# Performance work log

Measured on AMD Instinct MI355X. Metric: run time of the kernel, lower is better.

Reference implementation:

```python
import jax, jax.numpy as jnp
import numpy as np

H, D, Kd, Vd = 16, 1024, 64, 64
N, Mlen = 4096, 4096


def setup_inputs() -> dict:
    key = jax.random.key(0)
    ks = jax.random.split(key, 7)
    X = jax.random.normal(ks[0], (N, D), dtype=jnp.float32)
    M = jax.random.normal(ks[1], (Mlen, D), dtype=jnp.float32)
    mask = jax.random.randint(ks[2], (N, Mlen), 0, 2, dtype=jnp.int32)
    Wq = jax.random.normal(ks[3], (H, D, Kd), dtype=jnp.float32)
    Wk = jax.random.normal(ks[4], (H, D, Kd), dtype=jnp.float32)
    Wv = jax.random.normal(ks[5], (H, D, Vd), dtype=jnp.float32)
    Wo = jax.random.normal(ks[6], (H, Vd, D), dtype=jnp.float32)
    return {"X": X, "M": M, "mask": mask, "Wq": Wq, "Wk": Wk, "Wv": Wv, "Wo": Wo}


def reference(X, M, mask, Wq, Wk, Wv, Wo):
    # Projections: [h,n,k], [h,m,k], [h,m,v]
    Q = jnp.einsum('nd,hdk->hnk', X, Wq)
    K = jnp.einsum('md,hdk->hmk', M, Wk)
    V = jnp.einsum('md,hdv->hmv', M, Wv)
    # Masked attention (no scaling, matching the source)
    logits = jnp.einsum('hnk,hmk->hnm', Q, K)
    logits = jnp.where(mask[None, :, :] == 0, -jnp.inf, logits)
    weights = jax.nn.softmax(logits, axis=-1)
    O = jnp.einsum('hnm,hmv->hnv', weights, V)
    Y = jnp.einsum('hnv,hvd->nd', O, Wo)
    return Y
```

## Files before the change

kernel.cpp:

```cpp
#include <hip/hip_runtime.h>

typedef _Float16 half8 __attribute__((ext_vector_type(8)));
typedef _Float16 half4 __attribute__((ext_vector_type(4)));
typedef __fp16 fp16x2 __attribute__((ext_vector_type(2)));
typedef short short8 __attribute__((ext_vector_type(8)));
typedef short short4v __attribute__((ext_vector_type(4)));
typedef float floatx4 __attribute__((ext_vector_type(4)));

#define LOG2E 1.4426950408889634f

#define GLDS16(g, l) __builtin_amdgcn_global_load_lds( \
    (const __attribute__((address_space(1))) unsigned int*)(g), \
    (__attribute__((address_space(3))) unsigned int*)(l), 16, 0, 0)

static __device__ __forceinline__ short f2bf(float f){
  union { float f; unsigned u; } v; v.f = f;
  unsigned r = v.u + 0x7fffu + ((v.u >> 16) & 1u);
  return (short)(r >> 16);
}
static __device__ __forceinline__ float bf2f(short s){
  union { unsigned u; float f; } v; v.u = ((unsigned)(unsigned short)s) << 16;
  return v.f;
}

__global__ __launch_bounds__(256) void kconvA(const float* __restrict__ X,
                                              const float* __restrict__ Mm,
                                              short* __restrict__ XFh, short* __restrict__ XFl,
                                              short* __restrict__ MFh, short* __restrict__ MFl){
  int b = blockIdx.x;
  int t = threadIdx.x, w = t >> 6, l = t & 63, quad = l >> 4;
  int srcsel = b >> 8, ntile = b & 255;
  const float* A = srcsel ? Mm : X;
  short* oh = srcsel ? MFh : XFh;
  short* ol = srcsel ? MFl : XFl;
  int row = ntile*16 + (l & 15);
  #pragma unroll
  for (int i = 0; i < 8; i++){
    int kt = w*8 + i;
    const float* p = A + (size_t)row*1024 + kt*32 + quad*8;
    float4 v0 = *(const float4*)p, v1 = *(const float4*)(p + 4);
    float vv[8] = {v0.x,v0.y,v0.z,v0.w,v1.x,v1.y,v1.z,v1.w};
    short8 hh, ll;
    #pragma unroll
    for (int j = 0; j < 8; j++){
      short hb = f2bf(vv[j]); hh[j] = hb; ll[j] = f2bf(vv[j] - bf2f(hb));
    }
    size_t off = ((size_t)kt*256 + ntile)*512 + l*8;
    *(short8*)&oh[off] = hh;
    *(short8*)&ol[off] = ll;
  }
}

__global__ __launch_bounds__(256) void kconvW2(const float* __restrict__ Wq,
                                               const float* __restrict__ Wk,
                                               const float* __restrict__ Wv,
                                               short* __restrict__ WFh, short* __restrict__ WFl){
  __shared__ float T[128][68];
  int bidx = blockIdx.x, g = blockIdx.y;
  int mat = bidx >> 4, h = bidx & 15;
  const float* W = (mat == 0 ? Wq : (mat == 1 ? Wk : Wv)) + (size_t)h*65536;
  int t = threadIdx.x, w = t >> 6, l = t & 63, quad = (l >> 4) & 3, fl = l & 15;
  #pragma unroll
  for (int p = 0; p < 32; p++){
    int idx = p*256 + t, row = idx >> 6, col = idx & 63;
    T[row][col] = W[(size_t)(g*128 + row)*64 + col];
  }
  __syncthreads();
  for (int ktl = 0; ktl < 4; ktl++){
    short8 hh, ll;
    #pragma unroll
    for (int j = 0; j < 8; j++){
      float v = T[ktl*32 + quad*8 + j][w*16 + fl];
      short hb = f2bf(v); hh[j] = hb; ll[j] = f2bf(v - bf2f(hb));
    }
    size_t frag = ((size_t)bidx*32 + g*4 + ktl)*4 + w;
    *(short8*)&WFh[frag*512 + l*8] = hh;
    *(short8*)&WFl[frag*512 + l*8] = ll;
  }
}

__global__ __launch_bounds__(256) void kmaskpack(const int* __restrict__ mask,
                                                 unsigned* __restrict__ bits){
  int w = blockIdx.x * 256 + threadIdx.x;
  const int* p = mask + (size_t)w * 32;
  unsigned b = 0;
  #pragma unroll
  for (int i = 0; i < 32; i++) b |= (p[i] != 0) ? (1u << i) : 0u;
  bits[w] = b;
}

__global__ __launch_bounds__(256) void ktransw(const float* __restrict__ src,
                                               short* __restrict__ dsth,
                                               short* __restrict__ dstl,
                                               int R, int C){
  __shared__ float tile[32][33];
  size_t boff = (size_t)blockIdx.z * R * C;
  src += boff; dsth += boff; dstl += boff;
  int r0 = blockIdx.y*32, c0 = blockIdx.x*32;
  int t = threadIdx.x, tr = t >> 3, tc = (t & 7)*4;
  const float* s = src + (size_t)(r0 + tr)*C + c0 + tc;
  #pragma unroll
  for (int i = 0; i < 4; i++) tile[tr][tc + i] = s[i];
  __syncthreads();
  short* dh = dsth + (size_t)(c0 + tr)*R + r0 + tc;
  short* dl = dstl + (size_t)(c0 + tr)*R + r0 + tc;
  #pragma unroll
  for (int i = 0; i < 4; i++){
    float v = tile[tc + i][tr];
    short hb = f2bf(v);
    dh[i] = hb; dl[i] = f2bf(v - bf2f(hb));
  }
}

__global__ __launch_bounds__(256,3) void kproj3(
    const short* __restrict__ XFh, const short* __restrict__ XFl,
    const short* __restrict__ MFh, const short* __restrict__ MFl,
    const short* __restrict__ WFh, const short* __restrict__ WFl,
    _Float16* __restrict__ QFh, _Float16* __restrict__ QFl,
    _Float16* __restrict__ KFh, _Float16* __restrict__ KFl,
    _Float16* __restrict__ VF)
{
  __shared__ short AhL[4096], AlL[4096], BhL[4096], BlL[4096];
  int cb = blockIdx.x, rb = blockIdx.y;
  const bool fused = (cb >= 16);
  int h = fused ? (cb - 16) : cb;
  const short* Ah = fused ? MFh : XFh;
  const short* Al = fused ? MFl : XFl;
  int t = threadIdx.x, w = t >> 6, l = t & 63, quad = l >> 4, ln = l & 15;
  floatx4 acc[2][8] = {};
  for (int kt = 0; kt < 32; kt++){
    __syncthreads();
    size_t abase = ((size_t)kt*256 + rb*8)*512;
    #pragma unroll
    for (int i = 0; i < 2; i++){
      int cidx = i*256 + t;
      GLDS16(Ah + abase + cidx*8, &AhL[(i*256 + w*64)*8]);
      GLDS16(Al + abase + cidx*8, &AlL[(i*256 + w*64)*8]);
    }
    size_t bb0 = (((size_t)cb*32 + kt)*4)*512;
    GLDS16(WFh + bb0 + t*8, &BhL[(w*64)*8]);
    GLDS16(WFl + bb0 + t*8, &BlL[(w*64)*8]);
    if (fused){
      size_t bb1 = (((size_t)(cb + 16)*32 + kt)*4)*512;
      GLDS16(WFh + bb1 + t*8, &BhL[(256 + w*64)*8]);
      GLDS16(WFl + bb1 + t*8, &BlL[(256 + w*64)*8]);
    }
    __syncthreads();
    short8 ah[2], al[2];
    #pragma unroll
    for (int mt = 0; mt < 2; mt++){
      ah[mt] = *(short8*)&AhL[(w*2 + mt)*512 + l*8];
      al[mt] = *(short8*)&AlL[(w*2 + mt)*512 + l*8];
    }
    {
      short8 bh[4], bl[4];
      #pragma unroll
      for (int nt = 0; nt < 4; nt++){
        bh[nt] = *(short8*)&BhL[nt*512 + l*8];
        bl[nt] = *(short8*)&BlL[nt*512 + l*8];
      }
      #pragma unroll
      for (int mt = 0; mt < 2; mt++)
        #pragma unroll
        for (int nt = 0; nt < 4; nt++){
          acc[mt][nt] = __builtin_amdgcn_mfma_f32_16x16x32_bf16(ah[mt], bh[nt], acc[mt][nt], 0, 0, 0);
          acc[mt][nt] = __builtin_amdgcn_mfma_f32_16x16x32_bf16(ah[mt], bl[nt], acc[mt][nt], 0, 0, 0);
          acc[mt][nt] = __builtin_amdgcn_mfma_f32_16x16x32_bf16(al[mt], bh[nt], acc[mt][nt], 0, 0, 0);
        }
    }
    if (fused){
      short8 bh[4], bl[4];
      #pragma unroll
      for (int nt = 0; nt < 4; nt++){
        bh[nt] = *(short8*)&BhL[(4 + nt)*512 + l*8];
        bl[nt] = *(short8*)&BlL[(4 + nt)*512 + l*8];
      }
      #pragma unroll
      for (int mt = 0; mt < 2; mt++)
        #pragma unroll
        for (int nt = 0; nt < 4; nt++){
          acc[mt][4+nt] = __builtin_amdgcn_mfma_f32_16x16x32_bf16(ah[mt], bh[nt], acc[mt][4+nt], 0, 0, 0);
          acc[mt][4+nt] = __builtin_amdgcn_mfma_f32_16x16x32_bf16(ah[mt], bl[nt], acc[mt][4+nt], 0, 0, 0);
          acc[mt][4+nt] = __builtin_amdgcn_mfma_f32_16x16x32_bf16(al[mt], bh[nt], acc[mt][4+nt], 0, 0, 0);
        }
    }
  }
  int row0 = rb*128;
  if (!fused){
    #pragma unroll
    for (int mt = 0; mt < 2; mt++)
      #pragma unroll
      for (int nt = 0; nt < 4; nt++)
        #pragma unroll
        for (int rg = 0; rg < 4; rg++){
          int n = row0 + w*32 + mt*16 + quad*4 + rg;
          int c = nt*16 + ln;
          float v = acc[mt][nt][rg] * LOG2E;
          _Float16 hi = (_Float16)v;
          _Float16 lo = (_Float16)(v - (float)hi);
          int lane2 = (n & 15) + (((c >> 3) & 3) << 4);
          size_t off = (((size_t)h*256 + (n >> 4))*2 + (c >> 5))*512 + lane2*8 + (c & 7);
          QFh[off] = hi; QFl[off] = lo;
        }
  } else {
    #pragma unroll
    for (int mt = 0; mt < 2; mt++)
      #pragma unroll
      for (int nt = 0; nt < 4; nt++)
        #pragma unroll
        for (int rg = 0; rg < 4; rg++){
          int n = row0 + w*32 + mt*16 + quad*4 + rg;
          int c = nt*16 + ln;
          float v = acc[mt][nt][rg];
          _Float16 hi = (_Float16)v;
          _Float16 lo = (_Float16)(v - (float)hi);
          int lane2 = (n & 15) + (((c >> 3) & 3) << 4);
          size_t off = (((size_t)h*256 + (n >> 4))*2 + (c >> 5))*512 + lane2*8 + (c & 7);
          KFh[off] = hi; KFl[off] = lo;
        }
    #pragma unroll
    for (int mt = 0; mt < 2; mt++)
      #pragma unroll
      for (int ntv = 0; ntv < 4; ntv++){
        union { fp16x2 h2[2]; unsigned u2[2]; } pu;
        pu.h2[0] = __builtin_amdgcn_cvt_pkrtz(acc[mt][4+ntv][0], acc[mt][4+ntv][1]);
        pu.h2[1] = __builtin_amdgcn_cvt_pkrtz(acc[mt][4+ntv][2], acc[mt][4+ntv][3]);
        size_t base = (((size_t)h*32 + rb)*16 + ntv*4 + w)*512;
        *(uint2*)&VF[base + (quad*16 + ln)*8 + mt*4] = *(uint2*)&pu.u2[0];
      }
  }
}

__global__ __launch_bounds__(256,4) void kattn8(
    const _Float16* __restrict__ QFh, const _Float16* __restrict__ QFl,
    const _Float16* __restrict__ KFh, const _Float16* __restrict__ KFl,
    const _Float16* __restrict__ VF, const unsigned* __restrict__ bits,
    short* __restrict__ Ows)
{
  __shared__ _Float16 KBh[2][4096], KBl[2][4096], VB[4096];
  int bx = blockIdx.x, h = bx & 15, qb = bx >> 4, q0 = qb*64;
  int t = threadIdx.x, w = t >> 6, l = t & 63, quad = l >> 4, ln = l & 15;

  half8 qh[2], ql[2];
  #pragma unroll
  for (int kc = 0; kc < 2; kc++){
    size_t off = (((size_t)h*256 + qb*4 + w)*2 + kc)*512 + l*8;
    qh[kc] = *(const half8*)&QFh[off];
    ql[kc] = *(const half8*)&QFl[off];
  }

  floatx4 o[4] = {};
  float mst = -1e30f, lst = 0.f;

  const size_t hb = (size_t)h*262144;
  const int cidx0 = t, cidx1 = 256 + t;
  const int ld0 = (w*64)*8, ld1 = (256 + w*64)*8;

  {
    GLDS16(KFh + hb + cidx0*8, &KBh[0][ld0]);
    GLDS16(KFh + hb + cidx1*8, &KBh[0][ld1]);
    GLDS16(KFl + hb + cidx0*8, &KBl[0][ld0]);
    GLDS16(KFl + hb + cidx1*8, &KBl[0][ld1]);
    #pragma unroll
    for (int i = 0; i < 2; i++){
      int cidx = i*256 + t;
      int lu = cidx >> 6, uoff = (cidx & 63)*8;
      int gu = (lu >> 1)*4 + (lu & 1);
      GLDS16(VF + hb + (size_t)gu*512 + uoff, &VB[(i*256 + w*64)*8]);
    }
  }
  uint2 mwv = *(const uint2*)&bits[(size_t)(q0 + w*16 + ln)*128];
  __syncthreads();

  int cur = 0;
  for (int kt = 0; kt < 64; kt++){
    int ktn = (kt + 1) & 63;
    size_t kbn = hb + (size_t)ktn*4096;
    GLDS16(KFh + kbn + cidx0*8, &KBh[cur^1][ld0]);
    GLDS16(KFh + kbn + cidx1*8, &KBh[cur^1][ld1]);
    GLDS16(KFl + kbn + cidx0*8, &KBl[cur^1][ld0]);
    GLDS16(KFl + kbn + cidx1*8, &KBl[cur^1][ld1]);
    uint2 mwn = *(const uint2*)&bits[(size_t)(q0 + w*16 + ln)*128 + ktn*2];

    floatx4 st[4] = {};
    __builtin_amdgcn_s_setprio(1);
    #pragma unroll
    for (int kc = 0; kc < 2; kc++)
      #pragma unroll
      for (int m8 = 0; m8 < 4; m8++){
        half8 kh = *(half8*)&KBh[cur][(m8*2 + kc)*512 + l*8];
        half8 kl = *(half8*)&KBl[cur][(m8*2 + kc)*512 + l*8];
        st[m8] = __builtin_amdgcn_mfma_f32_16x16x32_f16(kh, qh[kc], st[m8], 0, 0, 0);
        st[m8] = __builtin_amdgcn_mfma_f32_16x16x32_f16(kl, qh[kc], st[m8], 0, 0, 0);
        st[m8] = __builtin_amdgcn_mfma_f32_16x16x32_f16(kh, ql[kc], st[m8], 0, 0, 0);
      }
    __builtin_amdgcn_s_setprio(0);

    {
      const unsigned mwp[2] = {mwv.x, mwv.y};
      #pragma unroll
      for (int m8 = 0; m8 < 4; m8++){
        unsigned nib = (mwp[m8 >> 1] >> ((m8 & 1)*16 + quad*4)) & 15u;
        #pragma unroll
        for (int rg = 0; rg < 4; rg++)
          if (!((nib >> rg) & 1u)) st[m8][rg] = -1e30f;
      }
      float a0 = fmaxf(fmaxf(st[0][0], st[0][1]), fmaxf(st[0][2], st[0][3]));
      float a1 = fmaxf(fmaxf(st[1][0], st[1][1]), fmaxf(st[1][2], st[1][3]));
      float a2 = fmaxf(fmaxf(st[2][0], st[2][1]), fmaxf(st[2][2], st[2][3]));
      float a3 = fmaxf(fmaxf(st[3][0], st[3][1]), fmaxf(st[3][2], st[3][3]));
      float mx = fmaxf(fmaxf(a0, a1), fmaxf(a2, a3));
      mx = fmaxf(mx, __shfl_xor(mx, 16));
      mx = fmaxf(mx, __shfl_xor(mx, 32));
      if (__any(mx > mst + 8.0f)){
        float mnew = fmaxf(mst, mx);
        float alpha = exp2f(mst - mnew);
        mst = mnew;
        lst *= alpha;
        #pragma unroll
        for (int vt = 0; vt < 4; vt++) o[vt] *= alpha;
      }
      float ssum = 0.f;
      #pragma unroll
      for (int m8 = 0; m8 < 4; m8++)
        #pragma unroll
        for (int rg = 0; rg < 4; rg++){
          float p = exp2f(st[m8][rg] - mst);
          st[m8][rg] = p; ssum += p;
        }
      lst += ssum;
    }
    mwv = mwn;

    __syncthreads();

    __builtin_amdgcn_s_setprio(1);
    #pragma unroll
    for (int p = 0; p < 2; p++){
      half8 vfp[4];
      #pragma unroll
      for (int vt = 0; vt < 4; vt++)
        vfp[vt] = *(half8*)&VB[((vt*2 + p)*512) + l*8];
      #pragma unroll
      for (int sub = 0; sub < 2; sub++){
        int m8 = p*2 + sub;
        union { fp16x2 h2[2]; half4 h4; } pu;
        pu.h2[0] = __builtin_amdgcn_cvt_pkrtz(st[m8][0], st[m8][1]);
        pu.h2[1] = __builtin_amdgcn_cvt_pkrtz(st[m8][2], st[m8][3]);
        #pragma unroll
        for (int vt = 0; vt < 4; vt++){
          half4 va = sub ? __builtin_shufflevector(vfp[vt], vfp[vt], 4,5,6,7)
                         : __builtin_shufflevector(vfp[vt], vfp[vt], 0,1,2,3);
          o[vt] = __builtin_amdgcn_mfma_f32_16x16x16f16(va, pu.h4, o[vt], 0, 0, 0);
        }
      }
    }
    __builtin_amdgcn_s_setprio(0);

    __syncthreads();

    {
      size_t vbn = hb + (size_t)(ktn >> 1)*8192;
      int vhalf = (ktn & 1)*2;
      #pragma unroll
      for (int i = 0; i < 2; i++){
        int cidx = i*256 + t;
        int lu = cidx >> 6, uoff = (cidx & 63)*8;
        int gu = (lu >> 1)*4 + vhalf + (lu & 1);
        GLDS16(VF + vbn + (size_t)gu*512 + uoff, &VB[(i*256 + w*64)*8]);
      }
    }
    cur ^= 1;
  }

  {
    lst += __shfl_xor(lst, 16);
    lst += __shfl_xor(lst, 32);
    float inv = (lst > 0.f) ? (1.f / lst) : 0.f;
    int n = q0 + w*16 + ln;
    #pragma unroll
    for (int vt = 0; vt < 4; vt++){
      short4v pk;
      #pragma unroll
      for (int rg = 0; rg < 4; rg++) pk[rg] = f2bf(o[vt][rg]*inv);
      *(short4v*)&Ows[(size_t)n*1024 + h*64 + vt*16 + quad*4] = pk;
    }
  }
}

__global__ __launch_bounds__(256,2) void kfinal(const short* __restrict__ Ain,
                                                const short* __restrict__ Bt,
                                                float* __restrict__ Y)
{
  __shared__ short Al[128*48];
  __shared__ short Bl[64*48];
  int cb = blockIdx.x, rb = blockIdx.y;
  int row0 = rb*128, col0 = cb*64;
  int t = threadIdx.x, w = t >> 6, l = t & 63, quad = l >> 4, ln = l & 15;
  floatx4 acc[2][4] = {};
  for (int d0 = 0; d0 < 1024; d0 += 32){
    #pragma unroll
    for (int i = 0; i < 2; i++){
      int u = t + i*256, r = u >> 2, s = u & 3;
      *(int4*)&Al[r*48 + s*8] = *(const int4*)&Ain[(size_t)(row0 + r)*1024 + d0 + s*8];
    }
    { int r = t >> 2, s = t & 3;
      *(int4*)&Bl[r*48 + s*8] = *(const int4*)&Bt[(size_t)(col0 + r)*1024 + d0 + s*8]; }
    __syncthreads();
    short8 bf[4];
    #pragma unroll
    for (int nt = 0; nt < 4; nt++) bf[nt] = *(short8*)&Bl[(nt*16 + ln)*48 + quad*8];
    #pragma unroll
    for (int mt = 0; mt < 2; mt++){
      short8 af = *(short8*)&Al[(w*32 + mt*16 + ln)*48 + quad*8];
      #pragma unroll
      for (int nt = 0; nt < 4; nt++)
        acc[mt][nt] = __builtin_amdgcn_mfma_f32_16x16x32_bf16(af, bf[nt], acc[mt][nt], 0, 0, 0);
    }
    __syncthreads();
  }
  #pragma unroll
  for (int mt = 0; mt < 2; mt++)
    #pragma unroll
    for (int nt = 0; nt < 4; nt++)
      #pragma unroll
      for (int rg = 0; rg < 4; rg++){
        int n = row0 + w*32 + mt*16 + quad*4 + rg;
        int c = col0 + nt*16 + ln;
        Y[(size_t)n*1024 + c] = acc[mt][nt][rg];
      }
}

extern "C" void kernel_launch(void* const* d_in, const int* in_sizes, int n_in,
                              void* d_out, int out_size, void* d_ws, size_t ws_size,
                              hipStream_t stream){
  (void)in_sizes; (void)n_in; (void)out_size; (void)ws_size;
  const float* X    = (const float*)d_in[0];
  const float* Mm   = (const float*)d_in[1];
  const int*   mask = (const int*)d_in[2];
  const float* Wq   = (const float*)d_in[3];
  const float* Wk   = (const float*)d_in[4];
  const float* Wv   = (const float*)d_in[5];
  const float* Wo   = (const float*)d_in[6];
  float* Y = (float*)d_out;
  char* ws = (char*)d_ws;
  const size_t MB = 1024*1024;
  short*    XFh   = (short*)   (ws +  0*MB);
  short*    XFl   = (short*)   (ws +  8*MB);
  short*    MFh   = (short*)   (ws + 16*MB);
  short*    MFl   = (short*)   (ws + 24*MB);
  short*    WFh   = (short*)   (ws + 32*MB);
  short*    WFl   = (short*)   (ws + 38*MB);
  unsigned* bits  = (unsigned*)(ws + 44*MB);
  _Float16* QFh   = (_Float16*)(ws + 46*MB);
  _Float16* QFl   = (_Float16*)(ws + 54*MB);
  _Float16* KFh   = (_Float16*)(ws + 62*MB);
  _Float16* KFl   = (_Float16*)(ws + 70*MB);
  _Float16* VF    = (_Float16*)(ws + 78*MB);
  short*    Ows   = (short*)   (ws +  0*MB);
  short*    Wot   = (short*)   (ws +  8*MB);
  short*    Wotl  = (short*)   (ws + 10*MB);

  kconvA<<<512, 256, 0, stream>>>(X, Mm, XFh, XFl, MFh, MFl);
  kconvW2<<<dim3(48,8), 256, 0, stream>>>(Wq, Wk, Wv, WFh, WFl);
  kmaskpack<<<2048, 256, 0, stream>>>(mask, bits);
  kproj3<<<dim3(32,32), 256, 0, stream>>>(XFh, XFl, MFh, MFl, WFh, WFl,
                                          QFh, QFl, KFh, KFl, VF);
  ktransw<<<dim3(32,32,1), 256, 0, stream>>>(Wo, Wot, Wotl, 1024, 1024);
  kattn8<<<1024, 256, 0, stream>>>(QFh, QFl, KFh, KFl, VF, bits, Ows);
  kfinal<<<dim3(16,32), 256, 0, stream>>>(Ows, Wot, Y);
}
```

Baseline: 459.0 us.

## Process two query tiles per wave in attention to reuse K/V LDS tiles

The attention kernel now gives each wave 32 query rows (two 16-row tiles) instead of 16, doubling the query block to 128 and halving the grid. The V tile is double-buffered like K, so only one barrier per key tile is needed instead of two. Each LDS K/V fragment read now feeds twice as many MFMAs, which cuts LDS and global traffic per unit of work. In exchange register pressure roughly doubles, launch bounds drop to 2 blocks per CU, and fewer blocks run, which may reduce latency hiding.

```diff
diff --git a/kernel.cpp b/kernel.cpp
--- a/kernel.cpp
+++ b/kernel.cpp
@@ -231,26 +231,28 @@
   }
 }
 
-__global__ __launch_bounds__(256,4) void kattn8(
+__global__ __launch_bounds__(256,2) void kattn9(
     const _Float16* __restrict__ QFh, const _Float16* __restrict__ QFl,
     const _Float16* __restrict__ KFh, const _Float16* __restrict__ KFl,
     const _Float16* __restrict__ VF, const unsigned* __restrict__ bits,
     short* __restrict__ Ows)
 {
-  __shared__ _Float16 KBh[2][4096], KBl[2][4096], VB[4096];
-  int bx = blockIdx.x, h = bx & 15, qb = bx >> 4, q0 = qb*64;
+  __shared__ _Float16 KBh[2][4096], KBl[2][4096], VB[2][4096];
+  int bx = blockIdx.x, h = bx & 15, qb = bx >> 4, q0 = qb*128;
   int t = threadIdx.x, w = t >> 6, l = t & 63, quad = l >> 4, ln = l & 15;
 
-  half8 qh[2], ql[2];
-  #pragma unroll
-  for (int kc = 0; kc < 2; kc++){
-    size_t off = (((size_t)h*256 + qb*4 + w)*2 + kc)*512 + l*8;
-    qh[kc] = *(const half8*)&QFh[off];
-    ql[kc] = *(const half8*)&QFl[off];
-  }
-
-  floatx4 o[4] = {};
-  float mst = -1e30f, lst = 0.f;
+  half8 qh[2][2], ql[2][2];
+  #pragma unroll
+  for (int nt2 = 0; nt2 < 2; nt2++)
+    #pragma unroll
+    for (int kc = 0; kc < 2; kc++){
+      size_t off = (((size_t)h*256 + qb*8 + w*2 + nt2)*2 + kc)*512 + l*8;
+      qh[nt2][kc] = *(const half8*)&QFh[off];
+      ql[nt2][kc] = *(const half8*)&QFl[off];
+    }
+
+  floatx4 o[2][4] = {};
+  float mst[2] = {-1e30f, -1e30f}, lst[2] = {0.f, 0.f};
 
   const size_t hb = (size_t)h*262144;
   const int cidx0 = t, cidx1 = 256 + t;
@@ -266,99 +268,19 @@
       int cidx = i*256 + t;
       int lu = cidx >> 6, uoff = (cidx & 63)*8;
       int gu = (lu >> 1)*4 + (lu & 1);
-      GLDS16(VF + hb + (size_t)gu*512 + uoff, &VB[(i*256 + w*64)*8]);
-    }
-  }
-  uint2 mwv = *(const uint2*)&bits[(size_t)(q0 + w*16 + ln)*128];
+      GLDS16(VF + hb + (size_t)gu*512 + uoff, &VB[0][(i*256 + w*64)*8]);
+    }
+  }
   __syncthreads();
 
   int cur = 0;
   for (int kt = 0; kt < 64; kt++){
-    int ktn = (kt + 1) & 63;
+    int ktn = (kt + 1) & 63, nxt = cur ^ 1;
     size_t kbn = hb + (size_t)ktn*4096;
-    GLDS16(KFh + kbn + cidx0*8, &KBh[cur^1][ld0]);
-    GLDS16(KFh + kbn + cidx1*8, &KBh[cur^1][ld1]);
-    GLDS16(KFl + kbn + cidx0*8, &KBl[cur^1][ld0]);
-    GLDS16(KFl + kbn + cidx1*8, &KBl[cur^1][ld1]);
-    uint2 mwn = *(const uint2*)&bits[(size_t)(q0 + w*16 + ln)*128 + ktn*2];
-
-    floatx4 st[4] = {};
-    __builtin_amdgcn_s_setprio(1);
-    #pragma unroll
-    for (int kc = 0; kc < 2; kc++)
-      #pragma unroll
-      for (int m8 = 0; m8 < 4; m8++){
-        half8 kh = *(half8*)&KBh[cur][(m8*2 + kc)*512 + l*8];
-        half8 kl = *(half8*)&KBl[cur][(m8*2 + kc)*512 + l*8];
-        st[m8] = __builtin_amdgcn_mfma_f32_16x16x32_f16(kh, qh[kc], st[m8], 0, 0, 0);
-        st[m8] = __builtin_amdgcn_mfma_f32_16x16x32_f16(kl, qh[kc], st[m8], 0, 0, 0);
-        st[m8] = __builtin_amdgcn_mfma_f32_16x16x32_f16(kh, ql[kc], st[m8], 0, 0, 0);
-      }
-    __builtin_amdgcn_s_setprio(0);
-
-    {
-      const unsigned mwp[2] = {mwv.x, mwv.y};
-      #pragma unroll
-      for (int m8 = 0; m8 < 4; m8++){
-        unsigned nib = (mwp[m8 >> 1] >> ((m8 & 1)*16 + quad*4)) & 15u;
-        #pragma unroll
-        for (int rg = 0; rg < 4; rg++)
-          if (!((nib >> rg) & 1u)) st[m8][rg] = -1e30f;
-      }
-      float a0 = fmaxf(fmaxf(st[0][0], st[0][1]), fmaxf(st[0][2], st[0][3]));
-      float a1 = fmaxf(fmaxf(st[1][0], st[1][1]), fmaxf(st[1][2], st[1][3]));
-      float a2 = fmaxf(fmaxf(st[2][0], st[2][1]), fmaxf(st[2][2], st[2][3]));
-      float a3 = fmaxf(fmaxf(st[3][0], st[3][1]), fmaxf(st[3][2], st[3][3]));
-      float mx = fmaxf(fmaxf(a0, a1), fmaxf(a2, a3));
-      mx = fmaxf(mx, __shfl_xor(mx, 16));
-      mx = fmaxf(mx, __shfl_xor(mx, 32));
-      if (__any(mx > mst + 8.0f)){
-        float mnew = fmaxf(mst, mx);
-        float alpha = exp2f(mst - mnew);
-        mst = mnew;
-        lst *= alpha;
-        #pragma unroll
-        for (int vt = 0; vt < 4; vt++) o[vt] *= alpha;
-      }
-      float ssum = 0.f;
-      #pragma unroll
-      for (int m8 = 0; m8 < 4; m8++)
-        #pragma unroll
-        for (int rg = 0; rg < 4; rg++){
-          float p = exp2f(st[m8][rg] - mst);
-          st[m8][rg] = p; ssum += p;
-        }
-      lst += ssum;
-    }
-    mwv = mwn;
-
-    __syncthreads();
-
-    __builtin_amdgcn_s_setprio(1);
-    #pragma unroll
-    for (int p = 0; p < 2; p++){
-      half8 vfp[4];
-      #pragma unroll
-      for (int vt = 0; vt < 4; vt++)
-        vfp[vt] = *(half8*)&VB[((vt*2 + p)*512) + l*8];
-      #pragma unroll
-      for (int sub = 0; sub < 2; sub++){
-        int m8 = p*2 + sub;
-        union { fp16x2 h2[2]; half4 h4; } pu;
-        pu.h2[0] = __builtin_amdgcn_cvt_pkrtz(st[m8][0], st[m8][1]);
-        pu.h2[1] = __builtin_amdgcn_cvt_pkrtz(st[m8][2], st[m8][3]);
-        #pragma unroll
-        for (int vt = 0; vt < 4; vt++){
-          half4 va = sub ? __builtin_shufflevector(vfp[vt], vfp[vt], 4,5,6,7)
-                         : __builtin_shufflevector(vfp[vt], vfp[vt], 0,1,2,3);
-          o[vt] = __builtin_amdgcn_mfma_f32_16x16x16f16(va, pu.h4, o[vt], 0, 0, 0);
-        }
-      }
-    }
-    __builtin_amdgcn_s_setprio(0);
-
-    __syncthreads();
-
+    GLDS16(KFh + kbn + cidx0*8, &KBh[nxt][ld0]);
+    GLDS16(KFh + kbn + cidx1*8, &KBh[nxt][ld1]);
+    GLDS16(KFl + kbn + cidx0*8, &KBl[nxt][ld0]);
+    GLDS16(KFl + kbn + cidx1*8, &KBl[nxt][ld1]);
     {
       size_t vbn = hb + (size_t)(ktn >> 1)*8192;
       int vhalf = (ktn & 1)*2;
@@ -367,22 +289,108 @@
         int cidx = i*256 + t;
         int lu = cidx >> 6, uoff = (cidx & 63)*8;
         int gu = (lu >> 1)*4 + vhalf + (lu & 1);
-        GLDS16(VF + vbn + (size_t)gu*512 + uoff, &VB[(i*256 + w*64)*8]);
-      }
-    }
-    cur ^= 1;
-  }
-
-  {
-    lst += __shfl_xor(lst, 16);
-    lst += __shfl_xor(lst, 32);
-    float inv = (lst > 0.f) ? (1.f / lst) : 0.f;
-    int n = q0 + w*16 + ln;
+        GLDS16(VF + vbn + (size_t)gu*512 + uoff, &VB[nxt][(i*256 + w*64)*8]);
+      }
+    }
+    uint2 mw[2];
+    mw[0] = *(const uint2*)&bits[(size_t)(q0 + w*32 + ln)*128 + kt*2];
+    mw[1] = *(const uint2*)&bits[(size_t)(q0 + w*32 + 16 + ln)*128 + kt*2];
+
+    floatx4 st[2][4] = {};
+    __builtin_amdgcn_s_setprio(1);
+    #pragma unroll
+    for (int kc = 0; kc < 2; kc++)
+      #pragma unroll
+      for (int m8 = 0; m8 < 4; m8++){
+        half8 kh = *(half8*)&KBh[cur][(m8*2 + kc)*512 + l*8];
+        half8 kl = *(half8*)&KBl[cur][(m8*2 + kc)*512 + l*8];
+        #pragma unroll
+        for (int nt2 = 0; nt2 < 2; nt2++){
+          st[nt2][m8] = __builtin_amdgcn_mfma_f32_16x16x32_f16(kh, qh[nt2][kc], st[nt2][m8], 0, 0, 0);
+          st[nt2][m8] = __builtin_amdgcn_mfma_f32_16x16x32_f16(kl, qh[nt2][kc], st[nt2][m8], 0, 0, 0);
+          st[nt2][m8] = __builtin_amdgcn_mfma_f32_16x16x32_f16(kh, ql[nt2][kc], st[nt2][m8], 0, 0, 0);
+        }
+      }
+    __builtin_amdgcn_s_setprio(0);
+
+    #pragma unroll
+    for (int nt2 = 0; nt2 < 2; nt2++){
+      const unsigned* mwp = (const unsigned*)&mw[nt2];
+      #pragma unroll
+      for (int m8 = 0; m8 < 4; m8++){
+        unsigned nib = (mwp[m8 >> 1] >> ((m8 & 1)*16 + quad*4)) & 15u;
+        #pragma unroll
+        for (int rg = 0; rg < 4; rg++)
+          if (!((nib >> rg) & 1u)) st[nt2][m8][rg] = -1e30f;
+      }
+      float a0 = fmaxf(fmaxf(st[nt2][0][0], st[nt2][0][1]), fmaxf(st[nt2][0][2], st[nt2][0][3]));
+      float a1 = fmaxf(fmaxf(st[nt2][1][0], st[nt2][1][1]), fmaxf(st[nt2][1][2], st[nt2][1][3]));
+      float a2 = fmaxf(fmaxf(st[nt2][2][0], st[nt2][2][1]), fmaxf(st[nt2][2][2], st[nt2][2][3]));
+      float a3 = fmaxf(fmaxf(st[nt2][3][0], st[nt2][3][1]), fmaxf(st[nt2][3][2], st[nt2][3][3]));
+      float mx = fmaxf(fmaxf(a0, a1), fmaxf(a2, a3));
+      mx = fmaxf(mx, __shfl_xor(mx, 16));
+      mx = fmaxf(mx, __shfl_xor(mx, 32));
+      if (__any(mx > mst[nt2] + 8.0f)){
+        float mnew = fmaxf(mst[nt2], mx);
+        float alpha = exp2f(mst[nt2] - mnew);
+        mst[nt2] = mnew;
+        lst[nt2] *= alpha;
+        #pragma unroll
+        for (int vt = 0; vt < 4; vt++) o[nt2][vt] *= alpha;
+      }
+      float ssum = 0.f;
+      #pragma unroll
+      for (int m8 = 0; m8 < 4; m8++)
+        #pragma unroll
+        for (int rg = 0; rg < 4; rg++){
+          float p = exp2f(st[nt2][m8][rg] - mst[nt2]);
+          st[nt2][m8][rg] = p; ssum += p;
+        }
+      lst[nt2] += ssum;
+    }
+
+    __builtin_amdgcn_s_setprio(1);
+    #pragma unroll
+    for (int p = 0; p < 2; p++){
+      half8 vfp[4];
+      #pragma unroll
+      for (int vt = 0; vt < 4; vt++)
+        vfp[vt] = *(half8*)&VB[cur][((vt*2 + p)*512) + l*8];
+      #pragma unroll
+      for (int sub = 0; sub < 2; sub++){
+        int m8 = p*2 + sub;
+        #pragma unroll
+        for (int nt2 = 0; nt2 < 2; nt2++){
+          union { fp16x2 h2[2]; half4 h4; } pu;
+          pu.h2[0] = __builtin_amdgcn_cvt_pkrtz(st[nt2][m8][0], st[nt2][m8][1]);
+          pu.h2[1] = __builtin_amdgcn_cvt_pkrtz(st[nt2][m8][2], st[nt2][m8][3]);
+          #pragma unroll
+          for (int vt = 0; vt < 4; vt++){
+            half4 va = sub ? __builtin_shufflevector(vfp[vt], vfp[vt], 4,5,6,7)
+                           : __builtin_shufflevector(vfp[vt], vfp[vt], 0,1,2,3);
+            o[nt2][vt] = __builtin_amdgcn_mfma_f32_16x16x16f16(va, pu.h4, o[nt2][vt], 0, 0, 0);
+          }
+        }
+      }
+    }
+    __builtin_amdgcn_s_setprio(0);
+
+    __syncthreads();
+    cur = nxt;
+  }
+
+  #pragma unroll
+  for (int nt2 = 0; nt2 < 2; nt2++){
+    float li = lst[nt2];
+    li += __shfl_xor(li, 16);
+    li += __shfl_xor(li, 32);
+    float inv = (li > 0.f) ? (1.f / li) : 0.f;
+    int n = q0 + w*32 + nt2*16 + ln;
     #pragma unroll
     for (int vt = 0; vt < 4; vt++){
       short4v pk;
       #pragma unroll
-      for (int rg = 0; rg < 4; rg++) pk[rg] = f2bf(o[vt][rg]*inv);
+      for (int rg = 0; rg < 4; rg++) pk[rg] = f2bf(o[nt2][vt][rg]*inv);
       *(short4v*)&Ows[(size_t)n*1024 + h*64 + vt*16 + quad*4] = pk;
     }
   }
@@ -467,6 +475,6 @@
   kproj3<<<dim3(32,32), 256, 0, stream>>>(XFh, XFl, MFh, MFl, WFh, WFl,
                                           QFh, QFl, KFh, KFl, VF);
   ktransw<<<dim3(32,32,1), 256, 0, stream>>>(Wo, Wot, Wotl, 1024, 1024);
-  kattn8<<<1024, 256, 0, stream>>>(QFh, QFl, KFh, KFl, VF, bits, Ows);
+  kattn9<<<512, 256, 0, stream>>>(QFh, QFl, KFh, KFl, VF, bits, Ows);
   kfinal<<<dim3(16,32), 256, 0, stream>>>(Ows, Wot, Y);
 }
```

Result: slower. 501.1 us (+9.2%).
